# Optimization experiments

Hardware: AMD Instinct MI355X
Metric: run time of the kernel (lower is better)

The kernel has to match this reference:

```python
import jax, jax.numpy as jnp
import numpy as np

COPIES = 4
OUT_BITS = 8
N = 2 ** OUT_BITS
IN_DIMS = 1024
BATCH = 256
CHANS = 2 * COPIES + 1  # skip=True


def setup_inputs() -> dict:
    key = jax.random.key(0)
    k1, k2 = jax.random.split(key)
    inp = jax.random.normal(k1, (BATCH, IN_DIMS), dtype=jnp.float32)
    # xavier-uniform-ish linear weight, zero bias
    fan = IN_DIMS + CHANS * N
    lim = np.sqrt(6.0 / fan)
    W_xy = jax.random.uniform(k2, (CHANS * N, IN_DIMS), dtype=jnp.float32, minval=-lim, maxval=lim)
    b_xy = jnp.zeros((CHANS * N,), dtype=jnp.float32)
    # Conv1d(copies+1, 1, 1) initialized to constant 1/(2*copies+1), zero bias
    w_out = jnp.full((COPIES + 1,), 1.0 / CHANS, dtype=jnp.float32)
    b_out = jnp.zeros((1,), dtype=jnp.float32)
    return {"input": inp, "W_xy": W_xy, "b_xy": b_xy, "w_out": w_out, "b_out": b_out}


def _soft_xor(x, y):
    # x, y: [M, N]; z[m, j] = logsumexp_i (x[m, i] + y[m, i ^ j])
    idx = jnp.arange(N)[:, None] ^ jnp.arange(N)[None, :]  # [N, N]
    return jax.nn.logsumexp(x[:, :, None] + y[:, idx], axis=1)  # [M, N]


def reference(input, W_xy, b_xy, w_out, b_out):
    B = input.shape[0]
    xy = input @ W_xy.T + b_xy                      # [B, CHANS*N]
    x = xy[:, : COPIES * N].reshape(B * COPIES, N)
    y = xy[:, COPIES * N : 2 * COPIES * N].reshape(B * COPIES, N)
    skip = xy[:, 2 * COPIES * N :].reshape(B, 1, N)
    z = _soft_xor(x, y).reshape(B, COPIES, N)
    z = jnp.concatenate([z, skip], axis=1)          # [B, COPIES+1, N]
    out = jnp.einsum("bcn,c->bn", z, w_out) + b_out  # 1x1 conv -> squeeze
    return out
```

## Files before the change

kernel.cpp:

```cpp
#include <hip/hip_runtime.h>
#include <hip/hip_bf16.h>

#define K_DIM   1024
#define N_OUT   256
#define XY_COLS 2304

typedef __bf16 bf16x4 __attribute__((ext_vector_type(4)));
typedef __bf16 bf16x8 __attribute__((ext_vector_type(8)));
typedef float  f32x4  __attribute__((ext_vector_type(4)));

__global__ __launch_bounds__(256) void gemm_xy_kernel(
    const float* __restrict__ A,
    const float* __restrict__ W,
    const float* __restrict__ bias,
    float* __restrict__ xy)
{
    const int t   = threadIdx.x;
    const int bid = blockIdx.x;
    const int mt  = bid / 36;
    const int nt  = bid - mt * 36;
    const int m0  = mt * 32;
    const int n0  = nt * 64;

    __shared__ __align__(16) __bf16 sA[32][32];
    __shared__ __align__(16) __bf16 sB[64][32];

    const int ra = t >> 3;
    const int ka = (t & 7) * 4;
    const int rw = t >> 2;
    const int kw = (t & 3) * 8;

    const float* pA = A + (m0 + ra) * K_DIM + ka;
    const float* pW = W + (n0 + rw) * K_DIM + kw;

    const int lane = t & 63;
    const int wv   = t >> 6;
    const int mh   = wv >> 1;
    const int nh   = wv & 1;
    const int l15  = lane & 15;
    const int quad = lane >> 4;

    f32x4 acc0 = {0.f, 0.f, 0.f, 0.f};
    f32x4 acc1 = {0.f, 0.f, 0.f, 0.f};

    float4 ar  = *(const float4*)pA;
    float4 wr0 = *(const float4*)pW;
    float4 wr1 = *(const float4*)(pW + 4);

    #pragma unroll 1
    for (int kk = 0; kk < K_DIM / 32; ++kk) {
        if (kk) __syncthreads();
        bf16x4 av = { (__bf16)ar.x, (__bf16)ar.y, (__bf16)ar.z, (__bf16)ar.w };
        *(bf16x4*)&sA[ra][ka] = av;
        bf16x8 wvec = { (__bf16)wr0.x, (__bf16)wr0.y, (__bf16)wr0.z, (__bf16)wr0.w,
                        (__bf16)wr1.x, (__bf16)wr1.y, (__bf16)wr1.z, (__bf16)wr1.w };
        *(bf16x8*)&sB[rw][kw] = wvec;
        if (kk + 1 < K_DIM / 32) {
            pA += 32; pW += 32;
            ar  = *(const float4*)pA;
            wr0 = *(const float4*)pW;
            wr1 = *(const float4*)(pW + 4);
        }
        __syncthreads();
        bf16x8 af  = *(bf16x8*)&sA[16 * mh + l15][quad * 8];
        bf16x8 bf0 = *(bf16x8*)&sB[32 * nh + l15][quad * 8];
        bf16x8 bf1 = *(bf16x8*)&sB[32 * nh + 16 + l15][quad * 8];
        acc0 = __builtin_amdgcn_mfma_f32_16x16x32_bf16(af, bf0, acc0, 0, 0, 0);
        acc1 = __builtin_amdgcn_mfma_f32_16x16x32_bf16(af, bf1, acc1, 0, 0, 0);
    }

    const int row0 = m0 + 16 * mh + quad * 4;
    const int col0 = n0 + 32 * nh + l15;
    const float b0 = bias[col0];
    const float b1 = bias[col0 + 16];
    #pragma unroll
    for (int r = 0; r < 4; ++r) {
        xy[(row0 + r) * XY_COLS + col0]      = acc0[r] + b0;
        xy[(row0 + r) * XY_COLS + col0 + 16] = acc1[r] + b1;
    }
}

__global__ __launch_bounds__(512) void softxor_kernel(
    const float* __restrict__ xy,
    const float* __restrict__ w_out,
    const float* __restrict__ b_out,
    float* __restrict__ out)
{
    const int b = blockIdx.x;
    const int t = threadIdx.x;

    __shared__ __align__(16) float ex[4][N_OUT];
    __shared__ __align__(16) float ey[4][N_OUT];
    __shared__ __align__(16) float sk[N_OUT];
    __shared__ __align__(16) float part[8][N_OUT];

    const float* row = xy + (long)b * XY_COLS;

    for (int e4 = t; e4 < XY_COLS / 4; e4 += 512) {
        float4 v = *(const float4*)(row + e4 * 4);
        int e = e4 * 4;
        if (e < 1024) {
            float* d = &ex[e >> 8][e & 255];
            d[0] = __expf(v.x); d[1] = __expf(v.y); d[2] = __expf(v.z); d[3] = __expf(v.w);
        } else if (e < 2048) {
            float* d = &ey[(e >> 8) - 4][e & 255];
            d[0] = __expf(v.x); d[1] = __expf(v.y); d[2] = __expf(v.z); d[3] = __expf(v.w);
        } else {
            float* d = &sk[e - 2048];
            d[0] = v.x; d[1] = v.y; d[2] = v.z; d[3] = v.w;
        }
    }
    __syncthreads();

    const int wv = t >> 6;
    const int c  = wv >> 1;
    const int h  = wv & 1;
    const int jh = t & 63;

    float S0 = 0.f, S1 = 0.f, S2 = 0.f, S3 = 0.f;
    const int ih0 = h * 32;
    #pragma unroll 4
    for (int ih = ih0; ih < ih0 + 32; ++ih) {
        float4 xa = *(const float4*)&ex[c][ih * 4];
        float4 yb = *(const float4*)&ey[c][(ih ^ jh) * 4];
        S0 += xa.x * yb.x + xa.y * yb.y + xa.z * yb.z + xa.w * yb.w;
        S1 += xa.x * yb.y + xa.y * yb.x + xa.z * yb.w + xa.w * yb.z;
        S2 += xa.x * yb.z + xa.y * yb.w + xa.z * yb.x + xa.w * yb.y;
        S3 += xa.x * yb.w + xa.y * yb.z + xa.z * yb.y + xa.w * yb.x;
    }
    *(float4*)&part[wv][jh * 4] = make_float4(S0, S1, S2, S3);
    __syncthreads();

    if (t < N_OUT) {
        float acc = w_out[4] * sk[t] + b_out[0];
        #pragma unroll
        for (int cc = 0; cc < 4; ++cc) {
            float S = part[2 * cc][t] + part[2 * cc + 1][t];
            acc += w_out[cc] * __logf(S);
        }
        out[b * N_OUT + t] = acc;
    }
}

extern "C" void kernel_launch(void* const* d_in, const int* in_sizes, int n_in,
                              void* d_out, int out_size, void* d_ws, size_t ws_size,
                              hipStream_t stream) {
    const float* input = (const float*)d_in[0];
    const float* W_xy  = (const float*)d_in[1];
    const float* b_xy  = (const float*)d_in[2];
    const float* w_out = (const float*)d_in[3];
    const float* b_out = (const float*)d_in[4];
    float* outp = (float*)d_out;
    float* xy   = (float*)d_ws;

    gemm_xy_kernel<<<288, 256, 0, stream>>>(input, W_xy, b_xy, xy);
    softxor_kernel<<<256, 512, 0, stream>>>(xy, w_out, b_out, outp);
}
```

Measured before the change: 92.54 us.

## Double-buffer GEMM LDS tiles with K=64 steps, XOR swizzle, and packed-FMA softxor

The GEMM kernel now stages K=64 per iteration into double-buffered LDS tiles and prefetches the next chunk's global loads into registers, which halves the iteration count and drops one barrier per step. LDS columns are XOR-swizzled by row to cut bank conflicts on the MFMA fragment reads. The softxor inner loop is rewritten as 2-wide float vectors so the compiler can emit packed FMA instructions. The costs are more registers and LDS per block, with a fully unrolled loop that grows code size.

```diff
diff --git a/kernel.cpp b/kernel.cpp
--- a/kernel.cpp
+++ b/kernel.cpp
@@ -5,9 +5,9 @@
 #define N_OUT   256
 #define XY_COLS 2304
 
-typedef __bf16 bf16x4 __attribute__((ext_vector_type(4)));
 typedef __bf16 bf16x8 __attribute__((ext_vector_type(8)));
 typedef float  f32x4  __attribute__((ext_vector_type(4)));
+typedef float  f32x2  __attribute__((ext_vector_type(2)));
 
 __global__ __launch_bounds__(256) void gemm_xy_kernel(
     const float* __restrict__ A,
@@ -22,16 +22,20 @@
     const int m0  = mt * 32;
     const int n0  = nt * 64;
 
-    __shared__ __align__(16) __bf16 sA[32][32];
-    __shared__ __align__(16) __bf16 sB[64][32];
+    __shared__ __align__(16) __bf16 sA[2][32][64];
+    __shared__ __align__(16) __bf16 sB[2][64][64];
 
     const int ra = t >> 3;
-    const int ka = (t & 7) * 4;
+    const int ka = (t & 7) * 8;
     const int rw = t >> 2;
-    const int kw = (t & 3) * 8;
+    const int kw = (t & 3) * 16;
 
     const float* pA = A + (m0 + ra) * K_DIM + ka;
     const float* pW = W + (n0 + rw) * K_DIM + kw;
+
+    const int kaS  = ka ^ ((ra & 7) * 8);
+    const int kwS0 = kw ^ ((rw & 7) * 8);
+    const int kwS1 = (kw + 8) ^ ((rw & 7) * 8);
 
     const int lane = t & 63;
     const int wv   = t >> 6;
@@ -40,33 +44,62 @@
     const int l15  = lane & 15;
     const int quad = lane >> 4;
 
+    const int arow  = 16 * mh + l15;
+    const int brow0 = 32 * nh + l15;
+    const int brow1 = brow0 + 16;
+    const int aswz  = (arow & 7) * 8;
+    const int bswz  = (brow0 & 7) * 8;
+
     f32x4 acc0 = {0.f, 0.f, 0.f, 0.f};
     f32x4 acc1 = {0.f, 0.f, 0.f, 0.f};
 
-    float4 ar  = *(const float4*)pA;
-    float4 wr0 = *(const float4*)pW;
-    float4 wr1 = *(const float4*)(pW + 4);
-
-    #pragma unroll 1
-    for (int kk = 0; kk < K_DIM / 32; ++kk) {
-        if (kk) __syncthreads();
-        bf16x4 av = { (__bf16)ar.x, (__bf16)ar.y, (__bf16)ar.z, (__bf16)ar.w };
-        *(bf16x4*)&sA[ra][ka] = av;
-        bf16x8 wvec = { (__bf16)wr0.x, (__bf16)wr0.y, (__bf16)wr0.z, (__bf16)wr0.w,
-                        (__bf16)wr1.x, (__bf16)wr1.y, (__bf16)wr1.z, (__bf16)wr1.w };
-        *(bf16x8*)&sB[rw][kw] = wvec;
-        if (kk + 1 < K_DIM / 32) {
-            pA += 32; pW += 32;
-            ar  = *(const float4*)pA;
-            wr0 = *(const float4*)pW;
-            wr1 = *(const float4*)(pW + 4);
+    float4 rA[2][2], rW[2][4];
+    rA[0][0] = *(const float4*)(pA);
+    rA[0][1] = *(const float4*)(pA + 4);
+    rW[0][0] = *(const float4*)(pW);
+    rW[0][1] = *(const float4*)(pW + 4);
+    rW[0][2] = *(const float4*)(pW + 8);
+    rW[0][3] = *(const float4*)(pW + 12);
+
+    #pragma unroll
+    for (int kk = 0; kk < 16; ++kk) {
+        const int buf = kk & 1;
+        const int nxt = buf ^ 1;
+        if (kk + 1 < 16) {
+            const float* qA = pA + (kk + 1) * 64;
+            const float* qW = pW + (kk + 1) * 64;
+            rA[nxt][0] = *(const float4*)(qA);
+            rA[nxt][1] = *(const float4*)(qA + 4);
+            rW[nxt][0] = *(const float4*)(qW);
+            rW[nxt][1] = *(const float4*)(qW + 4);
+            rW[nxt][2] = *(const float4*)(qW + 8);
+            rW[nxt][3] = *(const float4*)(qW + 12);
+        }
+        {
+            float4 a0 = rA[buf][0], a1 = rA[buf][1];
+            bf16x8 av = { (__bf16)a0.x, (__bf16)a0.y, (__bf16)a0.z, (__bf16)a0.w,
+                          (__bf16)a1.x, (__bf16)a1.y, (__bf16)a1.z, (__bf16)a1.w };
+            *(bf16x8*)&sA[buf][ra][kaS] = av;
+            float4 w0 = rW[buf][0], w1 = rW[buf][1];
+            float4 w2 = rW[buf][2], w3 = rW[buf][3];
+            bf16x8 wv0 = { (__bf16)w0.x, (__bf16)w0.y, (__bf16)w0.z, (__bf16)w0.w,
+                           (__bf16)w1.x, (__bf16)w1.y, (__bf16)w1.z, (__bf16)w1.w };
+            bf16x8 wv1 = { (__bf16)w2.x, (__bf16)w2.y, (__bf16)w2.z, (__bf16)w2.w,
+                           (__bf16)w3.x, (__bf16)w3.y, (__bf16)w3.z, (__bf16)w3.w };
+            *(bf16x8*)&sB[buf][rw][kwS0] = wv0;
+            *(bf16x8*)&sB[buf][rw][kwS1] = wv1;
         }
         __syncthreads();
-        bf16x8 af  = *(bf16x8*)&sA[16 * mh + l15][quad * 8];
-        bf16x8 bf0 = *(bf16x8*)&sB[32 * nh + l15][quad * 8];
-        bf16x8 bf1 = *(bf16x8*)&sB[32 * nh + 16 + l15][quad * 8];
-        acc0 = __builtin_amdgcn_mfma_f32_16x16x32_bf16(af, bf0, acc0, 0, 0, 0);
-        acc1 = __builtin_amdgcn_mfma_f32_16x16x32_bf16(af, bf1, acc1, 0, 0, 0);
+        bf16x8 af0 = *(const bf16x8*)&sA[buf][arow][(quad * 8)      ^ aswz];
+        bf16x8 af1 = *(const bf16x8*)&sA[buf][arow][(32 + quad * 8) ^ aswz];
+        bf16x8 b00 = *(const bf16x8*)&sB[buf][brow0][(quad * 8)      ^ bswz];
+        bf16x8 b01 = *(const bf16x8*)&sB[buf][brow0][(32 + quad * 8) ^ bswz];
+        bf16x8 b10 = *(const bf16x8*)&sB[buf][brow1][(quad * 8)      ^ bswz];
+        bf16x8 b11 = *(const bf16x8*)&sB[buf][brow1][(32 + quad * 8) ^ bswz];
+        acc0 = __builtin_amdgcn_mfma_f32_16x16x32_bf16(af0, b00, acc0, 0, 0, 0);
+        acc0 = __builtin_amdgcn_mfma_f32_16x16x32_bf16(af1, b01, acc0, 0, 0, 0);
+        acc1 = __builtin_amdgcn_mfma_f32_16x16x32_bf16(af0, b10, acc1, 0, 0, 0);
+        acc1 = __builtin_amdgcn_mfma_f32_16x16x32_bf16(af1, b11, acc1, 0, 0, 0);
     }
 
     const int row0 = m0 + 16 * mh + quad * 4;
@@ -117,18 +150,31 @@
     const int h  = wv & 1;
     const int jh = t & 63;
 
-    float S0 = 0.f, S1 = 0.f, S2 = 0.f, S3 = 0.f;
+    f32x2 s01 = {0.f, 0.f};
+    f32x2 s23 = {0.f, 0.f};
     const int ih0 = h * 32;
     #pragma unroll 4
     for (int ih = ih0; ih < ih0 + 32; ++ih) {
         float4 xa = *(const float4*)&ex[c][ih * 4];
         float4 yb = *(const float4*)&ey[c][(ih ^ jh) * 4];
-        S0 += xa.x * yb.x + xa.y * yb.y + xa.z * yb.z + xa.w * yb.w;
-        S1 += xa.x * yb.y + xa.y * yb.x + xa.z * yb.w + xa.w * yb.z;
-        S2 += xa.x * yb.z + xa.y * yb.w + xa.z * yb.x + xa.w * yb.y;
-        S3 += xa.x * yb.w + xa.y * yb.z + xa.z * yb.y + xa.w * yb.x;
-    }
-    *(float4*)&part[wv][jh * 4] = make_float4(S0, S1, S2, S3);
+        f32x2 yp0  = { yb.x, yb.y };
+        f32x2 yp0s = { yb.y, yb.x };
+        f32x2 yp1  = { yb.z, yb.w };
+        f32x2 yp1s = { yb.w, yb.z };
+        f32x2 xx = { xa.x, xa.x };
+        f32x2 xy2 = { xa.y, xa.y };
+        f32x2 xz = { xa.z, xa.z };
+        f32x2 xw = { xa.w, xa.w };
+        s01 += xx  * yp0;
+        s01 += xy2 * yp0s;
+        s01 += xz  * yp1;
+        s01 += xw  * yp1s;
+        s23 += xx  * yp1;
+        s23 += xy2 * yp1s;
+        s23 += xz  * yp0;
+        s23 += xw  * yp0s;
+    }
+    *(float4*)&part[wv][jh * 4] = make_float4(s01.x, s01.y, s23.x, s23.y);
     __syncthreads();
 
     if (t < N_OUT) {
```

Result: faster. 85.30 us (-7.8%).
